# Performance work log

Measured on AMD Instinct MI355X. Metric: run time of the kernel, lower is better.

Reference implementation:

```python
import jax, jax.numpy as jnp
import numpy as np

DIM = 1024
HEADS = 16
HEAD_DIM = DIM // HEADS
SCALE = HEAD_DIM ** -0.5
EPS = 1e-5


def layernorm(x, g, b):
    mu = jnp.mean(x, axis=-1, keepdims=True)
    var = jnp.mean((x - mu) ** 2, axis=-1, keepdims=True)
    return (x - mu) * jax.lax.rsqrt(var + EPS) * g + b


def setup_inputs() -> dict:
    key = jax.random.key(0)
    ks = jax.random.split(key, 12)
    B, N = 2, 2048
    s = DIM ** -0.5
    return {
        "q": jax.random.normal(ks[0], (B, N, DIM), jnp.float32),
        "k": jax.random.normal(ks[1], (B, N, DIM), jnp.float32),
        "v": jax.random.normal(ks[2], (B, N, DIM), jnp.float32),
        "gq": jnp.ones((DIM,), jnp.float32), "bq_ln": jnp.zeros((DIM,), jnp.float32),
        "gk": jnp.ones((DIM,), jnp.float32), "bk_ln": jnp.zeros((DIM,), jnp.float32),
        "gv": jnp.ones((DIM,), jnp.float32), "bv_ln": jnp.zeros((DIM,), jnp.float32),
        "Wq": jax.random.normal(ks[3], (DIM, DIM), jnp.float32) * s,
        "bq": jnp.zeros((DIM,), jnp.float32),
        "Wk": jax.random.normal(ks[4], (DIM, DIM), jnp.float32) * s,
        "bk": jnp.zeros((DIM,), jnp.float32),
        "Wv": jax.random.normal(ks[5], (DIM, DIM), jnp.float32) * s,
        "bv": jnp.zeros((DIM,), jnp.float32),
        "Wp": jax.random.normal(ks[6], (DIM, DIM), jnp.float32) * s,
        "bp": jnp.zeros((DIM,), jnp.float32),
    }


def reference(q, k, v, gq, bq_ln, gk, bk_ln, gv, bv_ln, Wq, bq, Wk, bk, Wv, bv, Wp, bp):
    B, Nq, C = q.shape
    Nk, Nv = k.shape[1], v.shape[1]
    qn = layernorm(q, gq, bq_ln)
    kn = layernorm(k, gk, bk_ln)
    vn = layernorm(v, gv, bv_ln)
    # project and split heads -> [B, H, N, hd]
    qh = (qn @ Wq + bq).reshape(B, Nq, HEADS, HEAD_DIM).transpose(0, 2, 1, 3)
    kh = (kn @ Wk + bk).reshape(B, Nk, HEADS, HEAD_DIM).transpose(0, 2, 1, 3)
    vh = (vn @ Wv + bv).reshape(B, Nv, HEADS, HEAD_DIM).transpose(0, 2, 1, 3)
    attn = jnp.einsum("bhqd,bhkd->bhqk", qh, kh) * SCALE
    attn = jax.nn.softmax(attn, axis=-1)
    out = jnp.einsum("bhqk,bhkd->bhqd", attn, vh)
    out = out.transpose(0, 2, 1, 3).reshape(B, Nq, C)
    out = out @ Wp + bp
    return (out, kh, vh)
```

## Files before the change

kernel.cpp:

```cpp
#include <hip/hip_runtime.h>
#include <cstdint>

#define DIMC 1024
#define NSEQ 2048
#define BATCH 2
#define HEADS 16
#define HD 64
#define MROWS (BATCH * NSEQ)

typedef unsigned short u16;
typedef unsigned int u32;
typedef __attribute__((ext_vector_type(8))) short bf16x8;
typedef __attribute__((ext_vector_type(4))) float f32x4;

#if __has_builtin(__builtin_amdgcn_exp2f)
#define EXP2(x) __builtin_amdgcn_exp2f(x)
#else
#define EXP2(x) exp2f(x)
#endif

__device__ __forceinline__ u16 f2bf(float f) {
  union { float f; u32 u; } v; v.f = f;
  u32 u = v.u;
  return (u16)((u + 0x7fffu + ((u >> 16) & 1u)) >> 16);
}
__device__ __forceinline__ u32 pack_rne(float a, float b) {
  return (u32)f2bf(a) | ((u32)f2bf(b) << 16);
}
__device__ __forceinline__ u32 pack_trunc(float a, float b) {
  union { float f; u32 u; } x, y; x.f = a; y.f = b;
  return (x.u >> 16) | (y.u & 0xffff0000u);
}
__device__ __forceinline__ void gload_lds16(const void* g, void* l) {
  __builtin_amdgcn_global_load_lds((const __attribute__((address_space(1))) void*)g,
                                   (__attribute__((address_space(3))) void*)l, 16, 0, 0);
}

__global__ __launch_bounds__(256)
void prep(const float* __restrict__ q, const float* __restrict__ k,
          const float* __restrict__ v,
          const float* __restrict__ gq, const float* __restrict__ bq,
          const float* __restrict__ gk, const float* __restrict__ bk,
          const float* __restrict__ gv, const float* __restrict__ bv,
          const float* __restrict__ w0, const float* __restrict__ w1,
          const float* __restrict__ w2, const float* __restrict__ w3,
          u16* __restrict__ xn, u16* __restrict__ wtout) {
  __shared__ float rs[4], rs2[4];
  __shared__ float tile[32][33];
  int tid = threadIdx.x;
  if (blockIdx.x < 3 * MROWS) {
    int rowid = blockIdx.x;
    int tensor = rowid >> 12;
    int r = rowid & 4095;
    const float *src, *g, *b;
    if (tensor == 0)      { src = q; g = gq; b = bq; }
    else if (tensor == 1) { src = k; g = gk; b = bk; }
    else                  { src = v; g = gv; b = bv; }
    src += (size_t)r * DIMC;
    u16* dst = xn + (size_t)tensor * MROWS * DIMC + (size_t)r * DIMC;
    float4 x = ((const float4*)src)[tid];
    float s  = x.x + x.y + x.z + x.w;
    float s2 = x.x*x.x + x.y*x.y + x.z*x.z + x.w*x.w;
    #pragma unroll
    for (int m = 1; m < 64; m <<= 1) { s += __shfl_xor(s, m); s2 += __shfl_xor(s2, m); }
    int wave = tid >> 6, lane = tid & 63;
    if (lane == 0) { rs[wave] = s; rs2[wave] = s2; }
    __syncthreads();
    s  = rs[0] + rs[1] + rs[2] + rs[3];
    s2 = rs2[0] + rs2[1] + rs2[2] + rs2[3];
    float mu  = s * (1.0f / DIMC);
    float var = s2 * (1.0f / DIMC) - mu * mu;
    float inv = rsqrtf(var + 1e-5f);
    float4 gg = ((const float4*)g)[tid];
    float4 bb = ((const float4*)b)[tid];
    uint2 o;
    o.x = pack_rne((x.x - mu) * inv * gg.x + bb.x, (x.y - mu) * inv * gg.y + bb.y);
    o.y = pack_rne((x.z - mu) * inv * gg.z + bb.z, (x.w - mu) * inv * gg.w + bb.w);
    ((uint2*)dst)[tid] = o;
  } else {
    int blk = blockIdx.x - 3 * MROWS;
    int widx = blk >> 10, t = blk & 1023;
    int ti = t >> 5, tj = t & 31;
    const float* W = (widx == 0) ? w0 : (widx == 1) ? w1 : (widx == 2) ? w2 : w3;
    u16* O = wtout + (size_t)widx * DIMC * DIMC;
    int tx = tid & 31, ty = tid >> 5;
    #pragma unroll
    for (int rr = 0; rr < 32; rr += 8)
      tile[ty + rr][tx] = W[(size_t)(ti * 32 + ty + rr) * DIMC + tj * 32 + tx];
    __syncthreads();
    #pragma unroll
    for (int rr = 0; rr < 32; rr += 8)
      O[(size_t)(tj * 32 + ty + rr) * DIMC + ti * 32 + tx] = f2bf(tile[tx][ty + rr]);
  }
}

__global__ __launch_bounds__(256)
void qkv_gemm(const u16* __restrict__ xn, const u16* __restrict__ wt,
              const float* __restrict__ bq, const float* __restrict__ bk,
              const float* __restrict__ bv,
              float* __restrict__ out, u16* __restrict__ qh,
              u16* __restrict__ khb, u16* __restrict__ vtb) {
  __shared__ u16 smem[128 * 136];
  u16* As = smem;
  u16* Bs = smem + 4096;
  u16* Ls = smem;
  const int z = blockIdx.z;
  const u16* A  = xn + (size_t)z * MROWS * DIMC;
  const u16* Bt = wt + (size_t)z * DIMC * DIMC;
  const float* bias = (z == 0) ? bq : (z == 1) ? bk : bv;
  const int bm = blockIdx.x, bn = blockIdx.y;
  const int tid = threadIdx.x;
  const int wave = tid >> 6, lane = tid & 63;
  const int wm = (wave & 1) * 64, wn = (wave >> 1) * 64;
  const int row = lane & 15, quad = lane >> 4;
  const float QSCL = 0.18033688011112042f;
  f32x4 acc[4][4] = {};
  for (int k0 = 0; k0 < DIMC; k0 += 32) {
    #pragma unroll
    for (int c = 0; c < 2; ++c) {
      int e = c * 2048 + tid * 8;
      int rr = e >> 5, col = e & 31;
      gload_lds16(&A[(size_t)(bm * 128 + rr) * DIMC + k0 + col], &As[e]);
      gload_lds16(&Bt[(size_t)(bn * 128 + rr) * DIMC + k0 + col], &Bs[e]);
    }
    __syncthreads();
    bf16x8 a[4], b[4];
    #pragma unroll
    for (int i = 0; i < 4; ++i)
      a[i] = *(const bf16x8*)(&As[(wm + i * 16 + row) * 32 + quad * 8]);
    #pragma unroll
    for (int j = 0; j < 4; ++j)
      b[j] = *(const bf16x8*)(&Bs[(wn + j * 16 + row) * 32 + quad * 8]);
    #pragma unroll
    for (int i = 0; i < 4; ++i)
      #pragma unroll
      for (int j = 0; j < 4; ++j)
        acc[i][j] = __builtin_amdgcn_mfma_f32_16x16x32_bf16(a[i], b[j], acc[i][j], 0, 0, 0);
    __syncthreads();
  }
  #pragma unroll
  for (int i = 0; i < 4; ++i) {
    #pragma unroll
    for (int j = 0; j < 4; ++j) {
      float val[4];
      #pragma unroll
      for (int r = 0; r < 4; ++r) {
        int m = bm * 128 + wm + i * 16 + quad * 4 + r;
        int c = bn * 128 + wn + j * 16 + row;
        val[r] = acc[i][j][r] + bias[c];
        int b_ = m >> 11, n = m & 2047, h = c >> 6, d = c & 63;
        int bh = b_ * HEADS + h;
        size_t hidx = ((size_t)bh * NSEQ + n) * HD + d;
        if (z == 0) {
          qh[hidx] = f2bf(val[r] * QSCL);
        } else {
          out[(size_t)z * MROWS * DIMC + hidx] = val[r];
          if (z == 1) khb[hidx] = f2bf(val[r]);
        }
      }
      if (z == 2) {
        int ct = wn + j * 16 + row;
        int mt = wm + i * 16 + quad * 4;
        u32* L = (u32*)(&Ls[ct * 136 + mt]);
        L[0] = pack_rne(val[0], val[1]);
        L[1] = pack_rne(val[2], val[3]);
      }
    }
  }
  if (z == 2) {
    __syncthreads();
    int b_ = (bm * 128) >> 11;
    int nbase = (bm * 128) & 2047;
    #pragma unroll
    for (int it = 0; it < 8; ++it) {
      int idx = it * 256 + tid;
      int ct = idx >> 4, ch = idx & 15;
      uint4 y = *(const uint4*)(&Ls[ct * 136 + ch * 8]);
      int c = bn * 128 + ct;
      int h = c >> 6, d = c & 63;
      size_t o = ((size_t)(b_ * HEADS + h) * HD + d) * NSEQ + nbase + ch * 8;
      *(uint4*)(&vtb[o]) = y;
    }
  }
}

__global__ __launch_bounds__(256)
void out_gemm(const u16* __restrict__ A, const u16* __restrict__ Bt,
              const float* __restrict__ bias, float* __restrict__ outf) {
  __shared__ u16 As[64 * 32];
  __shared__ u16 Bs[128 * 32];
  const int bm = blockIdx.x, bn = blockIdx.y;
  const int tid = threadIdx.x;
  const int wave = tid >> 6, lane = tid & 63;
  const int wm = (wave & 1) * 32, wn = (wave >> 1) * 64;
  const int row = lane & 15, quad = lane >> 4;
  f32x4 acc[2][4] = {};
  for (int k0 = 0; k0 < DIMC; k0 += 32) {
    {
      int e = tid * 8;
      int rr = e >> 5, col = e & 31;
      gload_lds16(&A[(size_t)(bm * 64 + rr) * DIMC + k0 + col], &As[e]);
    }
    #pragma unroll
    for (int c = 0; c < 2; ++c) {
      int e = c * 2048 + tid * 8;
      int rr = e >> 5, col = e & 31;
      gload_lds16(&Bt[(size_t)(bn * 128 + rr) * DIMC + k0 + col], &Bs[e]);
    }
    __syncthreads();
    bf16x8 a[2], b[4];
    #pragma unroll
    for (int i = 0; i < 2; ++i)
      a[i] = *(const bf16x8*)(&As[(wm + i * 16 + row) * 32 + quad * 8]);
    #pragma unroll
    for (int j = 0; j < 4; ++j)
      b[j] = *(const bf16x8*)(&Bs[(wn + j * 16 + row) * 32 + quad * 8]);
    #pragma unroll
    for (int i = 0; i < 2; ++i)
      #pragma unroll
      for (int j = 0; j < 4; ++j)
        acc[i][j] = __builtin_amdgcn_mfma_f32_16x16x32_bf16(a[i], b[j], acc[i][j], 0, 0, 0);
    __syncthreads();
  }
  #pragma unroll
  for (int i = 0; i < 2; ++i)
    #pragma unroll
    for (int j = 0; j < 4; ++j)
      #pragma unroll
      for (int r = 0; r < 4; ++r) {
        int m = bm * 64 + wm + i * 16 + quad * 4 + r;
        int c = bn * 128 + wn + j * 16 + row;
        outf[(size_t)m * DIMC + c] = acc[i][j][r] + bias[c];
      }
}

__global__ __launch_bounds__(256)
void attn_fused(const u16* __restrict__ qh, const u16* __restrict__ kh,
                const u16* __restrict__ vt, u16* __restrict__ ao) {
  __shared__ u16 Ks[128 * 64];
  __shared__ u16 Vs[64 * 128];
  __shared__ u16 Ps[4][16 * 40];
  const int qtile = blockIdx.x;
  const int bh = blockIdx.y;
  const int b = bh >> 4, h = bh & 15;
  const int tid = threadIdx.x;
  const int wave = tid >> 6, lane = tid & 63;
  const int qi = lane & 15, quad = lane >> 4;
  const int sw = qi & 7;
  const size_t base = (size_t)bh * NSEQ * HD;
  bf16x8 qf[2];
  {
    int qrow = qtile * 64 + wave * 16 + qi;
    #pragma unroll
    for (int kc = 0; kc < 2; ++kc)
      qf[kc] = *(const bf16x8*)(&qh[base + (size_t)qrow * HD + kc * 32 + quad * 8]);
  }
  float li = 0.f;
  f32x4 oacc[4] = {};
  u16* myPs = &Ps[wave][0];
  for (int kt = 0; kt < NSEQ / 128; ++kt) {
    __syncthreads();
    #pragma unroll
    for (int c = 0; c < 4; ++c) {
      int p = c * 256 + tid;
      int rk = p >> 3, ck = p & 7;
      gload_lds16(&kh[base + (size_t)(kt * 128 + rk) * HD + (ck ^ (rk & 7)) * 8], &Ks[p * 8]);
      int rv = p >> 4, cv = p & 15;
      gload_lds16(&vt[base + (size_t)rv * NSEQ + kt * 128 + (cv ^ (rv & 15)) * 8], &Vs[p * 8]);
    }
    __syncthreads();
    #pragma unroll
    for (int kc = 0; kc < 4; ++kc) {
      f32x4 s0 = {}, s1 = {};
      {
        const u16* kr0 = &Ks[((kc * 2) * 16 + qi) * 64];
        s0 = __builtin_amdgcn_mfma_f32_16x16x32_bf16(
            *(const bf16x8*)(&kr0[(quad ^ sw) * 8]), qf[0], s0, 0, 0, 0);
        s0 = __builtin_amdgcn_mfma_f32_16x16x32_bf16(
            *(const bf16x8*)(&kr0[((4 + quad) ^ sw) * 8]), qf[1], s0, 0, 0, 0);
        const u16* kr1 = &Ks[((kc * 2 + 1) * 16 + qi) * 64];
        s1 = __builtin_amdgcn_mfma_f32_16x16x32_bf16(
            *(const bf16x8*)(&kr1[(quad ^ sw) * 8]), qf[0], s1, 0, 0, 0);
        s1 = __builtin_amdgcn_mfma_f32_16x16x32_bf16(
            *(const bf16x8*)(&kr1[((4 + quad) ^ sw) * 8]), qf[1], s1, 0, 0, 0);
      }
      float p0 = EXP2(s0[0]), p1 = EXP2(s0[1]), p2 = EXP2(s0[2]), p3 = EXP2(s0[3]);
      float p4 = EXP2(s1[0]), p5 = EXP2(s1[1]), p6 = EXP2(s1[2]), p7 = EXP2(s1[3]);
      float psum = ((p0 + p1) + (p2 + p3)) + ((p4 + p5) + (p6 + p7));
      {
        u32* w0 = (u32*)(&myPs[qi * 40 + quad * 4]);
        w0[0] = pack_trunc(p0, p1);
        w0[1] = pack_trunc(p2, p3);
        u32* w1 = (u32*)(&myPs[qi * 40 + 16 + quad * 4]);
        w1[0] = pack_trunc(p4, p5);
        w1[1] = pack_trunc(p6, p7);
      }
      psum += __shfl_xor(psum, 16);
      psum += __shfl_xor(psum, 32);
      li += psum;
      asm volatile("" ::: "memory");
      bf16x8 pf = *(const bf16x8*)(&myPs[qi * 40 + quad * 8]);
      #pragma unroll
      for (int dt = 0; dt < 4; ++dt) {
        bf16x8 vf = *(const bf16x8*)(&Vs[(dt * 16 + qi) * 128 + ((kc * 4 + quad) ^ qi) * 8]);
        oacc[dt] = __builtin_amdgcn_mfma_f32_16x16x32_bf16(vf, pf, oacc[dt], 0, 0, 0);
      }
    }
  }
  {
    float inv = 1.0f / li;
    int token = b * NSEQ + qtile * 64 + wave * 16 + qi;
    #pragma unroll
    for (int dt = 0; dt < 4; ++dt) {
      int col = h * 64 + dt * 16 + quad * 4;
      *(u32*)(&ao[(size_t)token * DIMC + col])     = pack_rne(oacc[dt][0] * inv, oacc[dt][1] * inv);
      *(u32*)(&ao[(size_t)token * DIMC + col + 2]) = pack_rne(oacc[dt][2] * inv, oacc[dt][3] * inv);
    }
  }
}

extern "C" void kernel_launch(void* const* d_in, const int* in_sizes, int n_in,
                              void* d_out, int out_size, void* d_ws, size_t ws_size,
                              hipStream_t stream) {
  const float* q    = (const float*)d_in[0];
  const float* k    = (const float*)d_in[1];
  const float* v    = (const float*)d_in[2];
  const float* gq   = (const float*)d_in[3];
  const float* bqln = (const float*)d_in[4];
  const float* gk   = (const float*)d_in[5];
  const float* bkln = (const float*)d_in[6];
  const float* gv   = (const float*)d_in[7];
  const float* bvln = (const float*)d_in[8];
  const float* Wq   = (const float*)d_in[9];
  const float* bq   = (const float*)d_in[10];
  const float* Wk   = (const float*)d_in[11];
  const float* bk   = (const float*)d_in[12];
  const float* Wv   = (const float*)d_in[13];
  const float* bv   = (const float*)d_in[14];
  const float* Wp   = (const float*)d_in[15];
  const float* bp   = (const float*)d_in[16];
  float* out = (float*)d_out;

  char* ws = (char*)d_ws;
  u16* xn  = (u16*)(ws);
  u16* wt  = (u16*)(ws + (size_t)25165824);
  u16* qh  = (u16*)(ws + (size_t)33554432);
  u16* khb = (u16*)(ws + (size_t)41943040);
  u16* ao  = (u16*)(ws + (size_t)50331648);
  u16* vtb = (u16*)d_out;

  const size_t WEL = (size_t)DIMC * DIMC;

  prep<<<3 * MROWS + 4096, 256, 0, stream>>>(q, k, v, gq, bqln, gk, bkln, gv, bvln,
                                             Wq, Wk, Wv, Wp, xn, wt);
  qkv_gemm<<<dim3(MROWS / 128, DIMC / 128, 3), 256, 0, stream>>>(
      xn, wt, bq, bk, bv, out, qh, khb, vtb);
  attn_fused<<<dim3(NSEQ / 64, BATCH * HEADS), 256, 0, stream>>>(qh, khb, vtb, ao);
  out_gemm<<<dim3(MROWS / 64, DIMC / 128), 256, 0, stream>>>(ao, wt + 3 * WEL, bp, out);
}
```

Measured before the change: 251.3 us.

## Batch all QK^T MFMAs per key tile before softmax and PV

Restructures the attention inner loop so all eight 16-key score tiles are computed first, then exponentiated and written to a full 128-wide per-wave P buffer with an XOR swizzle, and only then consumed by the PV MFMAs. This is meant to expose more independent MFMA work and let the compiler overlap the score matmuls, exp and LDS traffic instead of running a serial dependency chain per 32-key chunk. It also does one cross-lane reduction per tile instead of four. In exchange it holds more accumulator registers live and uses a larger LDS P buffer, which may lower occupancy.

```diff
diff --git a/kernel.cpp b/kernel.cpp
--- a/kernel.cpp
+++ b/kernel.cpp
@@ -239,7 +239,7 @@
                 const u16* __restrict__ vt, u16* __restrict__ ao) {
   __shared__ u16 Ks[128 * 64];
   __shared__ u16 Vs[64 * 128];
-  __shared__ u16 Ps[4][16 * 40];
+  __shared__ u16 Ps[4][16 * 128];
   const int qtile = blockIdx.x;
   const int bh = blockIdx.y;
   const int b = bh >> 4, h = bh & 15;
@@ -269,40 +269,42 @@
       gload_lds16(&vt[base + (size_t)rv * NSEQ + kt * 128 + (cv ^ (rv & 15)) * 8], &Vs[p * 8]);
     }
     __syncthreads();
+    f32x4 s[8];
+    #pragma unroll
+    for (int nt = 0; nt < 8; ++nt) {
+      const u16* kr = &Ks[(nt * 16 + qi) * 64];
+      f32x4 a = {};
+      a = __builtin_amdgcn_mfma_f32_16x16x32_bf16(
+          *(const bf16x8*)(&kr[(quad ^ sw) * 8]), qf[0], a, 0, 0, 0);
+      a = __builtin_amdgcn_mfma_f32_16x16x32_bf16(
+          *(const bf16x8*)(&kr[((4 + quad) ^ sw) * 8]), qf[1], a, 0, 0, 0);
+      s[nt] = a;
+    }
+    float psum = 0.f;
+    u16* prow = &myPs[qi * 128];
+    #pragma unroll
+    for (int nt = 0; nt < 8; ++nt) {
+      float p0 = EXP2(s[nt][0]);
+      float p1 = EXP2(s[nt][1]);
+      float p2 = EXP2(s[nt][2]);
+      float p3 = EXP2(s[nt][3]);
+      psum += (p0 + p1) + (p2 + p3);
+      int chunk = (nt * 2 + (quad >> 1)) ^ qi;
+      u32* w = (u32*)(&prow[chunk * 8 + (quad & 1) * 4]);
+      w[0] = pack_trunc(p0, p1);
+      w[1] = pack_trunc(p2, p3);
+    }
+    psum += __shfl_xor(psum, 16);
+    psum += __shfl_xor(psum, 32);
+    li += psum;
+    asm volatile("" ::: "memory");
     #pragma unroll
     for (int kc = 0; kc < 4; ++kc) {
-      f32x4 s0 = {}, s1 = {};
-      {
-        const u16* kr0 = &Ks[((kc * 2) * 16 + qi) * 64];
-        s0 = __builtin_amdgcn_mfma_f32_16x16x32_bf16(
-            *(const bf16x8*)(&kr0[(quad ^ sw) * 8]), qf[0], s0, 0, 0, 0);
-        s0 = __builtin_amdgcn_mfma_f32_16x16x32_bf16(
-            *(const bf16x8*)(&kr0[((4 + quad) ^ sw) * 8]), qf[1], s0, 0, 0, 0);
-        const u16* kr1 = &Ks[((kc * 2 + 1) * 16 + qi) * 64];
-        s1 = __builtin_amdgcn_mfma_f32_16x16x32_bf16(
-            *(const bf16x8*)(&kr1[(quad ^ sw) * 8]), qf[0], s1, 0, 0, 0);
-        s1 = __builtin_amdgcn_mfma_f32_16x16x32_bf16(
-            *(const bf16x8*)(&kr1[((4 + quad) ^ sw) * 8]), qf[1], s1, 0, 0, 0);
-      }
-      float p0 = EXP2(s0[0]), p1 = EXP2(s0[1]), p2 = EXP2(s0[2]), p3 = EXP2(s0[3]);
-      float p4 = EXP2(s1[0]), p5 = EXP2(s1[1]), p6 = EXP2(s1[2]), p7 = EXP2(s1[3]);
-      float psum = ((p0 + p1) + (p2 + p3)) + ((p4 + p5) + (p6 + p7));
-      {
-        u32* w0 = (u32*)(&myPs[qi * 40 + quad * 4]);
-        w0[0] = pack_trunc(p0, p1);
-        w0[1] = pack_trunc(p2, p3);
-        u32* w1 = (u32*)(&myPs[qi * 40 + 16 + quad * 4]);
-        w1[0] = pack_trunc(p4, p5);
-        w1[1] = pack_trunc(p6, p7);
-      }
-      psum += __shfl_xor(psum, 16);
-      psum += __shfl_xor(psum, 32);
-      li += psum;
-      asm volatile("" ::: "memory");
-      bf16x8 pf = *(const bf16x8*)(&myPs[qi * 40 + quad * 8]);
+      int pc = ((kc * 4 + quad) ^ qi) * 8;
+      bf16x8 pf = *(const bf16x8*)(&prow[pc]);
       #pragma unroll
       for (int dt = 0; dt < 4; ++dt) {
-        bf16x8 vf = *(const bf16x8*)(&Vs[(dt * 16 + qi) * 128 + ((kc * 4 + quad) ^ qi) * 8]);
+        bf16x8 vf = *(const bf16x8*)(&Vs[(dt * 16 + qi) * 128 + pc]);
         oacc[dt] = __builtin_amdgcn_mfma_f32_16x16x32_bf16(vf, pf, oacc[dt], 0, 0, 0);
       }
     }
```

New measurement: 264.7 us. 1.05x slower.
